# Kernel optimization log

Hardware: AMD Instinct MI355X
Metric: run time of the kernel (lower is better)

The kernel has to match this reference:

```python
import jax, jax.numpy as jnp
import numpy as np

NV, NE = 4096, 8192
FV, FE = 128, 64
FV_OUT = 128


def setup_inputs() -> dict:
    key = jax.random.key(0)
    ks = jax.random.split(key, 8)
    stdv = 1.0 / np.sqrt(FV_OUT)
    return {
        "H_v": jax.random.normal(ks[0], (NV, FV), dtype=jnp.float32),
        "H_e": jax.random.normal(ks[1], (NE, FE), dtype=jnp.float32),
        "adj_e": jax.random.uniform(ks[2], (NE, NE), dtype=jnp.float32),
        "adj_v": jax.random.uniform(ks[3], (NV, NV), dtype=jnp.float32),
        "T": jax.random.uniform(ks[4], (NV, NE), dtype=jnp.float32),
        "weight": jax.random.uniform(ks[5], (FV, FV_OUT), minval=-stdv, maxval=stdv, dtype=jnp.float32),
        "p": jax.random.normal(ks[6], (1, FE), dtype=jnp.float32),
        "bias": jax.random.uniform(ks[7], (FV_OUT,), minval=-stdv, maxval=stdv, dtype=jnp.float32),
    }


def reference(H_v, H_e, adj_e, adj_v, T, weight, p, bias):
    # node_layer=True path of GraphConvolution.forward
    # d = (H_e @ p.T) as a vector over edges; T @ diag(d) == T * d[None, :]
    d = (H_e @ p.T)[:, 0]                       # [Ne]
    multiplier = (T * d[None, :]) @ T.T         # [Nv, Nv]
    n = multiplier.shape[0]
    mask = jnp.eye(n, dtype=multiplier.dtype)   # eye mask: diag -> 1, off-diag -> multiplier
    M1 = mask + (1.0 - mask) * multiplier
    adjusted_A = M1 * adj_v                     # elementwise mask with dense adjacency
    output = adjusted_A @ (H_v @ weight) + bias # [Nv, Fv_out]
    return (output, H_e)
```

## Files before the change

### kernel.cpp

```cpp
#include <hip/hip_runtime.h>
#include <stdint.h>

#define NV 4096
#define NE 8192
#define FV 128
#define FE 64
#define FOUT 128

typedef unsigned short u16;
typedef __attribute__((ext_vector_type(8))) short short8;
typedef __attribute__((ext_vector_type(4))) float f32x4;
typedef __attribute__((ext_vector_type(4))) unsigned short u16x4;

__device__ __forceinline__ u16 f2bf(float f) {
  uint32_t u = __builtin_bit_cast(uint32_t, f);
  u += 0x7fffu + ((u >> 16) & 1u);
  return (u16)(u >> 16);
}
__device__ __forceinline__ float bf2f(u16 h) {
  return __builtin_bit_cast(float, (uint32_t)h << 16);
}

#define AS1(p) ((__attribute__((address_space(1))) void*)(void*)(p))
#define AS3(p) ((__attribute__((address_space(3))) void*)(p))

__device__ __forceinline__ void tri_decode(int id, int& bi, int& bj) {
  bi = (int)((sqrtf(8.0f * (float)id + 1.0f) - 1.0f) * 0.5f);
  while ((bi + 1) * (bi + 2) / 2 <= id) ++bi;
  while (bi * (bi + 1) / 2 > id) --bi;
  bj = id - bi * (bi + 1) / 2;
}

__global__ __launch_bounds__(64) void k_edge_dot(const float* __restrict__ He,
                                                 const float* __restrict__ p,
                                                 float* __restrict__ d) {
  int e = blockIdx.x;
  int l = threadIdx.x;
  float v = He[e * FE + l] * p[l];
  #pragma unroll
  for (int off = 32; off > 0; off >>= 1) v += __shfl_down(v, off);
  if (l == 0) d[e] = v;
}

__global__ __launch_bounds__(256) void k_convert(const float* __restrict__ T,
                                                 const float* __restrict__ d,
                                                 u16* __restrict__ Ta,
                                                 u16* __restrict__ Tb) {
  size_t idx = ((size_t)blockIdx.x * 256 + threadIdx.x) * 4;
  f32x4 t = *(const f32x4*)&T[idx];
  int e = (int)(idx & (NE - 1));
  f32x4 dv = *(const f32x4*)&d[e];
  u16x4 a, b;
  a.x = f2bf(t.x * dv.x); a.y = f2bf(t.y * dv.y);
  a.z = f2bf(t.z * dv.z); a.w = f2bf(t.w * dv.w);
  b.x = f2bf(t.x); b.y = f2bf(t.y); b.z = f2bf(t.z); b.w = f2bf(t.w);
  *(u16x4*)&Ta[idx] = a;
  *(u16x4*)&Tb[idx] = b;
}

__global__ __launch_bounds__(128) void k_hw(const float* __restrict__ Hv,
                                            const float* __restrict__ W,
                                            u16* __restrict__ HWt) {
  __shared__ float sh[FV];
  int i = blockIdx.x;
  int n = threadIdx.x;
  sh[n] = Hv[i * FV + n];
  __syncthreads();
  float s = 0.f;
  #pragma unroll
  for (int f = 0; f < FV; ++f) s += sh[f] * W[f * FOUT + n];
  HWt[(size_t)n * NV + i] = f2bf(s);
}

__global__ __launch_bounds__(256) void k_init_out(float* __restrict__ out,
                                                  const float* __restrict__ bias,
                                                  const float* __restrict__ He) {
  int idx = blockIdx.x * 256 + threadIdx.x;
  if (idx < NV * FOUT) out[idx] = bias[idx & (FOUT - 1)];
  else out[idx] = He[idx - NV * FOUT];
}

__global__ __launch_bounds__(256) void k_gemm_sym(const u16* __restrict__ Ta,
                                                  const u16* __restrict__ Tb,
                                                  u16* __restrict__ Mp) {
  __shared__ __align__(16) u16 lA[128 * 32];
  __shared__ __align__(16) u16 lB[128 * 32];
  const int bx = blockIdx.x;
  const int pair = bx >> 1;
  const int split = bx & 1;
  int bi, bj;
  tri_decode(pair, bi, bj);

  const int K = NE;
  const int kbeg = split * (K / 2);
  const int kend = kbeg + K / 2;
  const int tile_m = bi * 128;
  const int tile_n = bj * 128;
  const int tid = threadIdx.x;
  const int lane = tid & 63;
  const int wave = tid >> 6;
  const int wm = (wave >> 1) * 64;
  const int wn = (wave & 1) * 64;
  const int row16 = lane & 15;
  const int quad = lane >> 4;

  f32x4 acc[4][4] = {};

  for (int k0 = kbeg; k0 < kend; k0 += 32) {
    __syncthreads();
    #pragma unroll
    for (int r = 0; r < 2; ++r) {
      const int chunk = r * 256 + wave * 64 + lane;
      const int row = chunk >> 2;
      const int cc = chunk & 3;
      const u16* ga = Ta + ((size_t)(tile_m + row) * K + k0 + cc * 8);
      const u16* gb = Tb + ((size_t)(tile_n + row) * K + k0 + cc * 8);
      __builtin_amdgcn_global_load_lds(AS1(ga), AS3(&lA[(r * 256 + wave * 64) * 8]), 16, 0, 0);
      __builtin_amdgcn_global_load_lds(AS1(gb), AS3(&lB[(r * 256 + wave * 64) * 8]), 16, 0, 0);
    }
    __syncthreads();
    short8 a[4], b[4];
    #pragma unroll
    for (int mi = 0; mi < 4; ++mi)
      a[mi] = *(const short8*)&lA[(wm + mi * 16 + row16) * 32 + quad * 8];
    #pragma unroll
    for (int ni = 0; ni < 4; ++ni)
      b[ni] = *(const short8*)&lB[(wn + ni * 16 + row16) * 32 + quad * 8];
    #pragma unroll
    for (int mi = 0; mi < 4; ++mi)
      #pragma unroll
      for (int ni = 0; ni < 4; ++ni)
        acc[mi][ni] = __builtin_amdgcn_mfma_f32_16x16x32_bf16(a[mi], b[ni], acc[mi][ni], 0, 0, 0);
  }

  u16* dst = Mp + (size_t)bx * 16384 + wave * 4096;
  #pragma unroll
  for (int mi = 0; mi < 4; ++mi) {
    #pragma unroll
    for (int ni = 0; ni < 4; ++ni) {
      const int f = mi * 4 + ni;
      u16x4 pk;
      pk.x = f2bf(acc[mi][ni][0]); pk.y = f2bf(acc[mi][ni][1]);
      pk.z = f2bf(acc[mi][ni][2]); pk.w = f2bf(acc[mi][ni][3]);
      *(u16x4*)&dst[f * 256 + lane * 4] = pk;
    }
  }
}

__global__ __launch_bounds__(256) void k_mask(const u16* __restrict__ Mp,
                                              const float* __restrict__ adjv,
                                              u16* __restrict__ adjA) {
  __shared__ __align__(16) u16 sT[128 * 136];
  const int pair = blockIdx.x;
  int bi, bj;
  tri_decode(pair, bi, bj);
  const int tile_m = bi * 128;
  const int tile_n = bj * 128;
  const int tid = threadIdx.x;
  const int lane = tid & 63;
  const int wave = tid >> 6;
  const int wm = (wave >> 1) * 64;
  const int wn = (wave & 1) * 64;
  const int row16 = lane & 15;
  const int quad = lane >> 4;

  const u16* s0 = Mp + (size_t)(pair * 2) * 16384 + wave * 4096;
  const u16* s1 = s0 + 16384;

  f32x4 acc[4][4];
  #pragma unroll
  for (int mi = 0; mi < 4; ++mi) {
    #pragma unroll
    for (int ni = 0; ni < 4; ++ni) {
      const int f = mi * 4 + ni;
      u16x4 a = *(const u16x4*)&s0[f * 256 + lane * 4];
      u16x4 b = *(const u16x4*)&s1[f * 256 + lane * 4];
      acc[mi][ni][0] = bf2f(a.x) + bf2f(b.x);
      acc[mi][ni][1] = bf2f(a.y) + bf2f(b.y);
      acc[mi][ni][2] = bf2f(a.z) + bf2f(b.z);
      acc[mi][ni][3] = bf2f(a.w) + bf2f(b.w);
    }
  }

  #pragma unroll
  for (int mi = 0; mi < 4; ++mi) {
    #pragma unroll
    for (int ni = 0; ni < 4; ++ni) {
      const int gc = tile_n + wn + ni * 16 + row16;
      #pragma unroll
      for (int r = 0; r < 4; ++r) {
        const int gr = tile_m + wm + mi * 16 + quad * 4 + r;
        float v = acc[mi][ni][r];
        if (gr == gc) v = 1.0f;
        v *= adjv[(size_t)gr * NV + gc];
        adjA[(size_t)gr * NV + gc] = f2bf(v);
      }
    }
  }

  if (bi != bj) {
    #pragma unroll
    for (int mi = 0; mi < 4; ++mi) {
      #pragma unroll
      for (int ni = 0; ni < 4; ++ni) {
        const int c = wn + ni * 16 + row16;
        const int r0 = wm + mi * 16 + quad * 4;
        u16x4 pk;
        pk.x = f2bf(acc[mi][ni][0]); pk.y = f2bf(acc[mi][ni][1]);
        pk.z = f2bf(acc[mi][ni][2]); pk.w = f2bf(acc[mi][ni][3]);
        *(u16x4*)&sT[c * 136 + r0] = pk;
      }
    }
    __syncthreads();
    const int row = tid >> 1;
    const int half = tid & 1;
    const size_t obase = (size_t)(tile_n + row) * NV + tile_m + half * 64;
    const u16* srow = &sT[row * 136 + half * 64];
    #pragma unroll
    for (int j = 0; j < 8; ++j) {
      short8 m8 = *(const short8*)&srow[j * 8];
      short8 o8;
      #pragma unroll
      for (int k = 0; k < 8; ++k) {
        float v = bf2f((u16)m8[k]) * adjv[obase + j * 8 + k];
        o8[k] = (short)f2bf(v);
      }
      *(short8*)&adjA[obase + j * 8] = o8;
    }
  }
}

#define KSPLIT 16
__global__ __launch_bounds__(256) void k_gemm_out(const u16* __restrict__ A,
                                                  const u16* __restrict__ B,
                                                  float* __restrict__ out) {
  __shared__ __align__(16) u16 lA[128 * 32];
  __shared__ __align__(16) u16 lB[128 * 32];
  const int K = NV;
  const int tile_m = blockIdx.y * 128;
  const int kbeg = blockIdx.x * (K / KSPLIT);
  const int kend = kbeg + (K / KSPLIT);
  const int tid = threadIdx.x;
  const int lane = tid & 63;
  const int wave = tid >> 6;
  const int wm = (wave >> 1) * 64;
  const int wn = (wave & 1) * 64;
  const int row16 = lane & 15;
  const int quad = lane >> 4;

  f32x4 acc[4][4] = {};

  for (int k0 = kbeg; k0 < kend; k0 += 32) {
    __syncthreads();
    #pragma unroll
    for (int r = 0; r < 2; ++r) {
      const int chunk = r * 256 + wave * 64 + lane;
      const int row = chunk >> 2;
      const int cc = chunk & 3;
      const u16* ga = A + ((size_t)(tile_m + row) * K + k0 + cc * 8);
      const u16* gb = B + ((size_t)row * K + k0 + cc * 8);
      __builtin_amdgcn_global_load_lds(AS1(ga), AS3(&lA[(r * 256 + wave * 64) * 8]), 16, 0, 0);
      __builtin_amdgcn_global_load_lds(AS1(gb), AS3(&lB[(r * 256 + wave * 64) * 8]), 16, 0, 0);
    }
    __syncthreads();
    short8 a[4], b[4];
    #pragma unroll
    for (int mi = 0; mi < 4; ++mi)
      a[mi] = *(const short8*)&lA[(wm + mi * 16 + row16) * 32 + quad * 8];
    #pragma unroll
    for (int ni = 0; ni < 4; ++ni)
      b[ni] = *(const short8*)&lB[(wn + ni * 16 + row16) * 32 + quad * 8];
    #pragma unroll
    for (int mi = 0; mi < 4; ++mi)
      #pragma unroll
      for (int ni = 0; ni < 4; ++ni)
        acc[mi][ni] = __builtin_amdgcn_mfma_f32_16x16x32_bf16(a[mi], b[ni], acc[mi][ni], 0, 0, 0);
  }

  #pragma unroll
  for (int mi = 0; mi < 4; ++mi) {
    #pragma unroll
    for (int ni = 0; ni < 4; ++ni) {
      const int gc = wn + ni * 16 + row16;
      #pragma unroll
      for (int r = 0; r < 4; ++r) {
        const int gr = tile_m + wm + mi * 16 + quad * 4 + r;
        atomicAdd(&out[(size_t)gr * FOUT + gc], acc[mi][ni][r]);
      }
    }
  }
}

extern "C" void kernel_launch(void* const* d_in, const int* in_sizes, int n_in,
                              void* d_out, int out_size, void* d_ws, size_t ws_size,
                              hipStream_t stream) {
  const float* Hv   = (const float*)d_in[0];
  const float* He   = (const float*)d_in[1];
  const float* adjv = (const float*)d_in[3];
  const float* T    = (const float*)d_in[4];
  const float* W    = (const float*)d_in[5];
  const float* p    = (const float*)d_in[6];
  const float* bias = (const float*)d_in[7];
  float* out = (float*)d_out;

  char* ws = (char*)d_ws;
  float* dvec = (float*)ws;
  u16* HWt  = (u16*)(ws + ((size_t)1 << 20));
  u16* Ta   = (u16*)(ws + ((size_t)2 << 20));
  u16* Tb   = (u16*)(ws + ((size_t)2 << 20) + ((size_t)64 << 20));
  u16* adjA = (u16*)(ws + ((size_t)2 << 20) + ((size_t)128 << 20));
  u16* Mp   = (u16*)(ws + ((size_t)2 << 20) + ((size_t)160 << 20));

  k_edge_dot<<<NE, 64, 0, stream>>>(He, p, dvec);
  k_convert<<<(NV * NE) / (256 * 4), 256, 0, stream>>>(T, dvec, Ta, Tb);
  k_hw<<<NV, 128, 0, stream>>>(Hv, W, HWt);
  k_init_out<<<(NV * FOUT + NE * FE) / 256, 256, 0, stream>>>(out, bias, He);
  k_gemm_sym<<<528 * 2, 256, 0, stream>>>(Ta, Tb, Mp);
  k_mask<<<528, 256, 0, stream>>>(Mp, adjv, adjA);
  k_gemm_out<<<dim3(KSPLIT, NV / 128), 256, 0, stream>>>(adjA, HWt, out);
}
```

Baseline: 735.7 us.

## Replace symmetric split-K GEMM and mask pass with fused pipelined 256x256 GEMM

Replaces the triangular split-K GEMM, which wrote bf16 partials, and the separate mask kernel with a single kernel. That kernel computes full 256x256 output tiles and applies the eye/adjacency mask in its epilogue. The main loop uses a multi-buffered LDS pipeline with asynchronous global-to-LDS loads, a swizzled LDS layout, explicit waitcnt and barrier scheduling, and raised wave priority around the MFMA bursts. This removes the round trip through the partial buffer, the extra launch and the transposed mirror writes. In exchange it gives up the symmetry saving and so roughly doubles the MFMA work for this product.

```diff
diff --git a/kernel.cpp b/kernel.cpp
--- a/kernel.cpp
+++ b/kernel.cpp
@@ -23,13 +23,6 @@
 
 #define AS1(p) ((__attribute__((address_space(1))) void*)(void*)(p))
 #define AS3(p) ((__attribute__((address_space(3))) void*)(p))
-
-__device__ __forceinline__ void tri_decode(int id, int& bi, int& bj) {
-  bi = (int)((sqrtf(8.0f * (float)id + 1.0f) - 1.0f) * 0.5f);
-  while ((bi + 1) * (bi + 2) / 2 <= id) ++bi;
-  while (bi * (bi + 1) / 2 > id) --bi;
-  bj = id - bi * (bi + 1) / 2;
-}
 
 __global__ __launch_bounds__(64) void k_edge_dot(const float* __restrict__ He,
                                                  const float* __restrict__ p,
@@ -80,154 +73,166 @@
   else out[idx] = He[idx - NV * FOUT];
 }
 
-__global__ __launch_bounds__(256) void k_gemm_sym(const u16* __restrict__ Ta,
-                                                  const u16* __restrict__ Tb,
-                                                  u16* __restrict__ Mp) {
-  __shared__ __align__(16) u16 lA[128 * 32];
-  __shared__ __align__(16) u16 lB[128 * 32];
-  const int bx = blockIdx.x;
-  const int pair = bx >> 1;
-  const int split = bx & 1;
-  int bi, bj;
-  tri_decode(pair, bi, bj);
-
-  const int K = NE;
-  const int kbeg = split * (K / 2);
-  const int kend = kbeg + K / 2;
-  const int tile_m = bi * 128;
-  const int tile_n = bj * 128;
+__global__ __launch_bounds__(512, 2) void k_gemm_m(const u16* __restrict__ Ta,
+                                                   const u16* __restrict__ Tb,
+                                                   const float* __restrict__ adjv,
+                                                   u16* __restrict__ adjA) {
+  __shared__ __align__(16) u16 smem[65536];
+
+  const int bi = blockIdx.x >> 4;
+  const int bj = blockIdx.x & 15;
+  const int tile_m = bi * 256;
+  const int tile_n = bj * 256;
   const int tid = threadIdx.x;
   const int lane = tid & 63;
-  const int wave = tid >> 6;
-  const int wm = (wave >> 1) * 64;
-  const int wn = (wave & 1) * 64;
+  const int wid = tid >> 6;
+  const int wr = wid >> 2;
+  const int wc = wid & 3;
   const int row16 = lane & 15;
   const int quad = lane >> 4;
-
-  f32x4 acc[4][4] = {};
-
-  for (int k0 = kbeg; k0 < kend; k0 += 32) {
-    __syncthreads();
-    #pragma unroll
-    for (int r = 0; r < 2; ++r) {
-      const int chunk = r * 256 + wave * 64 + lane;
-      const int row = chunk >> 2;
-      const int cc = chunk & 3;
-      const u16* ga = Ta + ((size_t)(tile_m + row) * K + k0 + cc * 8);
-      const u16* gb = Tb + ((size_t)(tile_n + row) * K + k0 + cc * 8);
-      __builtin_amdgcn_global_load_lds(AS1(ga), AS3(&lA[(r * 256 + wave * 64) * 8]), 16, 0, 0);
-      __builtin_amdgcn_global_load_lds(AS1(gb), AS3(&lB[(r * 256 + wave * 64) * 8]), 16, 0, 0);
-    }
-    __syncthreads();
-    short8 a[4], b[4];
-    #pragma unroll
-    for (int mi = 0; mi < 4; ++mi)
-      a[mi] = *(const short8*)&lA[(wm + mi * 16 + row16) * 32 + quad * 8];
-    #pragma unroll
-    for (int ni = 0; ni < 4; ++ni)
-      b[ni] = *(const short8*)&lB[(wn + ni * 16 + row16) * 32 + quad * 8];
-    #pragma unroll
-    for (int mi = 0; mi < 4; ++mi)
-      #pragma unroll
-      for (int ni = 0; ni < 4; ++ni)
-        acc[mi][ni] = __builtin_amdgcn_mfma_f32_16x16x32_bf16(a[mi], b[ni], acc[mi][ni], 0, 0, 0);
+  const int swz8 = (quad ^ ((row16 >> 1) & 3)) * 8;
+
+  const int srow = tid >> 2;
+  const int sslot = (tid & 3) ^ ((tid >> 3) & 3);
+  const u16* gA0 = Ta + (size_t)(tile_m + srow) * NE + sslot * 8;
+  const u16* gA1 = gA0 + (size_t)128 * NE;
+  const u16* gB0 = Tb + (size_t)(tile_n + srow) * NE + sslot * 8;
+  const u16* gB1 = gB0 + (size_t)128 * NE;
+  const int ldsO0 = (wid * 64) * 8;
+  const int ldsO1 = (512 + wid * 64) * 8;
+
+#define STG(gp0, gp1, roff, kcol)                                                                 \
+  do {                                                                                            \
+    __builtin_amdgcn_global_load_lds(AS1((gp0) + (kcol)), AS3(&smem[(roff) + ldsO0]), 16, 0, 0);  \
+    __builtin_amdgcn_global_load_lds(AS1((gp1) + (kcol)), AS3(&smem[(roff) + ldsO1]), 16, 0, 0);  \
+  } while (0)
+
+  f32x4 acc[8][4] = {};
+  short8 aF[8], bF[2];
+
+  const int arow32 = (wr * 128 + row16) * 32 + swz8;
+  const int brow32 = (wc * 64 + row16) * 32 + swz8;
+
+#define LDA(b, kk)                                                                \
+  do { _Pragma("unroll")                                                          \
+    for (int mi = 0; mi < 8; ++mi)                                                \
+      aF[mi] = *(const short8*)&smem[(b)*16384 + (kk)*8192 + arow32 + mi * 512];  \
+  } while (0)
+
+#define LDB(b, kk, nh)                                                                             \
+  do { _Pragma("unroll")                                                                           \
+    for (int nn = 0; nn < 2; ++nn)                                                                 \
+      bF[nn] = *(const short8*)&smem[32768 + (b)*16384 + (kk)*8192 + brow32 + ((nh)*2+nn) * 512];  \
+  } while (0)
+
+#define MM(nh)                                                                                              \
+  do { _Pragma("unroll")                                                                                    \
+    for (int mi = 0; mi < 8; ++mi) {                                                                        \
+      acc[mi][(nh)*2+0] = __builtin_amdgcn_mfma_f32_16x16x32_bf16(aF[mi], bF[0], acc[mi][(nh)*2+0], 0,0,0); \
+      acc[mi][(nh)*2+1] = __builtin_amdgcn_mfma_f32_16x16x32_bf16(aF[mi], bF[1], acc[mi][(nh)*2+1], 0,0,0); \
+    }                                                                                                       \
+  } while (0)
+
+#define BAR()   __builtin_amdgcn_s_barrier()
+#define LGKM0() do { asm volatile("s_waitcnt lgkmcnt(0)" ::: "memory"); \
+                     __builtin_amdgcn_sched_barrier(0); } while (0)
+#define VM6()   asm volatile("s_waitcnt vmcnt(6)" ::: "memory")
+#define PRIO1() __builtin_amdgcn_s_setprio(1)
+#define PRIO0() __builtin_amdgcn_s_setprio(0)
+
+  STG(gA0, gA1, 0,             0);
+  STG(gB0, gB1, 32768,         0);
+  STG(gA0, gA1, 8192,          32);
+  STG(gB0, gB1, 32768 + 8192,  32);
+  STG(gA0, gA1, 16384,         64);
+  STG(gB0, gB1, 32768 + 16384, 64);
+  STG(gA0, gA1, 16384 + 8192,  96);
+  VM6();
+  BAR();
+
+  for (int it = 0; it < 64; ++it) {
+    const int t = it * 2;
+    const int k1 = (t + 1) * 64;
+    const int k2 = (t + 2 < 128 ? t + 2 : 127) * 64;
+    const int k3 = (t + 3 < 128 ? t + 3 : 127) * 64;
+
+    LDA(0, 0); LDB(0, 0, 0);
+    STG(gB0, gB1, 32768 + 16384 + 8192, k1 + 32);
+    BAR(); LGKM0();
+    PRIO1(); MM(0); PRIO0();
+    BAR();
+
+    LDB(0, 0, 1);
+    STG(gA0, gA1, 0, k2);
+    BAR(); LGKM0();
+    PRIO1(); MM(1); PRIO0();
+    BAR();
+
+    LDA(0, 1); LDB(0, 1, 0);
+    STG(gB0, gB1, 32768, k2);
+    BAR(); LGKM0();
+    PRIO1(); MM(0); PRIO0();
+    BAR();
+
+    LDB(0, 1, 1);
+    STG(gA0, gA1, 8192, k2 + 32);
+    BAR(); LGKM0();
+    PRIO1(); MM(1); PRIO0();
+    VM6();
+    BAR();
+
+    LDA(1, 0); LDB(1, 0, 0);
+    STG(gB0, gB1, 32768 + 8192, k2 + 32);
+    BAR(); LGKM0();
+    PRIO1(); MM(0); PRIO0();
+    BAR();
+
+    LDB(1, 0, 1);
+    STG(gA0, gA1, 16384, k3);
+    BAR(); LGKM0();
+    PRIO1(); MM(1); PRIO0();
+    BAR();
+
+    LDA(1, 1); LDB(1, 1, 0);
+    STG(gB0, gB1, 32768 + 16384, k3);
+    BAR(); LGKM0();
+    PRIO1(); MM(0); PRIO0();
+    BAR();
+
+    LDB(1, 1, 1);
+    STG(gA0, gA1, 16384 + 8192, k3 + 32);
+    BAR(); LGKM0();
+    PRIO1(); MM(1); PRIO0();
+    VM6();
+    BAR();
   }
 
-  u16* dst = Mp + (size_t)bx * 16384 + wave * 4096;
   #pragma unroll
-  for (int mi = 0; mi < 4; ++mi) {
+  for (int mi = 0; mi < 8; ++mi) {
+    const int gr0 = tile_m + wr * 128 + mi * 16 + quad * 4;
     #pragma unroll
     for (int ni = 0; ni < 4; ++ni) {
-      const int f = mi * 4 + ni;
-      u16x4 pk;
-      pk.x = f2bf(acc[mi][ni][0]); pk.y = f2bf(acc[mi][ni][1]);
-      pk.z = f2bf(acc[mi][ni][2]); pk.w = f2bf(acc[mi][ni][3]);
-      *(u16x4*)&dst[f * 256 + lane * 4] = pk;
-    }
-  }
-}
-
-__global__ __launch_bounds__(256) void k_mask(const u16* __restrict__ Mp,
-                                              const float* __restrict__ adjv,
-                                              u16* __restrict__ adjA) {
-  __shared__ __align__(16) u16 sT[128 * 136];
-  const int pair = blockIdx.x;
-  int bi, bj;
-  tri_decode(pair, bi, bj);
-  const int tile_m = bi * 128;
-  const int tile_n = bj * 128;
-  const int tid = threadIdx.x;
-  const int lane = tid & 63;
-  const int wave = tid >> 6;
-  const int wm = (wave >> 1) * 64;
-  const int wn = (wave & 1) * 64;
-  const int row16 = lane & 15;
-  const int quad = lane >> 4;
-
-  const u16* s0 = Mp + (size_t)(pair * 2) * 16384 + wave * 4096;
-  const u16* s1 = s0 + 16384;
-
-  f32x4 acc[4][4];
-  #pragma unroll
-  for (int mi = 0; mi < 4; ++mi) {
-    #pragma unroll
-    for (int ni = 0; ni < 4; ++ni) {
-      const int f = mi * 4 + ni;
-      u16x4 a = *(const u16x4*)&s0[f * 256 + lane * 4];
-      u16x4 b = *(const u16x4*)&s1[f * 256 + lane * 4];
-      acc[mi][ni][0] = bf2f(a.x) + bf2f(b.x);
-      acc[mi][ni][1] = bf2f(a.y) + bf2f(b.y);
-      acc[mi][ni][2] = bf2f(a.z) + bf2f(b.z);
-      acc[mi][ni][3] = bf2f(a.w) + bf2f(b.w);
-    }
-  }
-
-  #pragma unroll
-  for (int mi = 0; mi < 4; ++mi) {
-    #pragma unroll
-    for (int ni = 0; ni < 4; ++ni) {
-      const int gc = tile_n + wn + ni * 16 + row16;
+      const int gc = tile_n + wc * 64 + ni * 16 + row16;
       #pragma unroll
       for (int r = 0; r < 4; ++r) {
-        const int gr = tile_m + wm + mi * 16 + quad * 4 + r;
+        const int gr = gr0 + r;
         float v = acc[mi][ni][r];
-        if (gr == gc) v = 1.0f;
+        v = (gr == gc) ? 1.0f : v;
         v *= adjv[(size_t)gr * NV + gc];
         adjA[(size_t)gr * NV + gc] = f2bf(v);
       }
     }
   }
 
-  if (bi != bj) {
-    #pragma unroll
-    for (int mi = 0; mi < 4; ++mi) {
-      #pragma unroll
-      for (int ni = 0; ni < 4; ++ni) {
-        const int c = wn + ni * 16 + row16;
-        const int r0 = wm + mi * 16 + quad * 4;
-        u16x4 pk;
-        pk.x = f2bf(acc[mi][ni][0]); pk.y = f2bf(acc[mi][ni][1]);
-        pk.z = f2bf(acc[mi][ni][2]); pk.w = f2bf(acc[mi][ni][3]);
-        *(u16x4*)&sT[c * 136 + r0] = pk;
-      }
-    }
-    __syncthreads();
-    const int row = tid >> 1;
-    const int half = tid & 1;
-    const size_t obase = (size_t)(tile_n + row) * NV + tile_m + half * 64;
-    const u16* srow = &sT[row * 136 + half * 64];
-    #pragma unroll
-    for (int j = 0; j < 8; ++j) {
-      short8 m8 = *(const short8*)&srow[j * 8];
-      short8 o8;
-      #pragma unroll
-      for (int k = 0; k < 8; ++k) {
-        float v = bf2f((u16)m8[k]) * adjv[obase + j * 8 + k];
-        o8[k] = (short)f2bf(v);
-      }
-      *(short8*)&adjA[obase + j * 8] = o8;
-    }
-  }
+#undef STG
+#undef LDA
+#undef LDB
+#undef MM
+#undef BAR
+#undef LGKM0
+#undef VM6
+#undef PRIO1
+#undef PRIO0
 }
 
 #define KSPLIT 16
@@ -309,13 +314,11 @@
   u16* Ta   = (u16*)(ws + ((size_t)2 << 20));
   u16* Tb   = (u16*)(ws + ((size_t)2 << 20) + ((size_t)64 << 20));
   u16* adjA = (u16*)(ws + ((size_t)2 << 20) + ((size_t)128 << 20));
-  u16* Mp   = (u16*)(ws + ((size_t)2 << 20) + ((size_t)160 << 20));
 
   k_edge_dot<<<NE, 64, 0, stream>>>(He, p, dvec);
   k_convert<<<(NV * NE) / (256 * 4), 256, 0, stream>>>(T, dvec, Ta, Tb);
   k_hw<<<NV, 128, 0, stream>>>(Hv, W, HWt);
   k_init_out<<<(NV * FOUT + NE * FE) / 256, 256, 0, stream>>>(out, bias, He);
-  k_gemm_sym<<<528 * 2, 256, 0, stream>>>(Ta, Tb, Mp);
-  k_mask<<<528, 256, 0, stream>>>(Mp, adjv, adjA);
+  k_gemm_m<<<256, 512, 0, stream>>>(Ta, Tb, adjv, adjA);
   k_gemm_out<<<dim3(KSPLIT, NV / 128), 256, 0, stream>>>(adjA, HWt, out);
 }
```

Measured after the change: 720.0 us. 1.02x faster.
